# Kernel tuning notes

Measured on AMD Instinct MI355X. Metric: run time of the kernel, lower is better.

The kernel has to match this reference:

```python
import jax, jax.numpy as jnp
import numpy as np

# Model dims (match init_kwargs / input_specs)
L, D, H, F = 4, 1024, 16, 4096   # layers, d_model, heads, ffn hidden
B, S = 4, 1024                    # batch, seq_len
HD = D // H                       # head dim = 64
K = 8                             # context-mask band width (k=8, 2//k == 0)
LN_EPS = 1e-5


def setup_inputs():
    key = jax.random.key(0)
    ks = jax.random.split(key, 16)
    s = 0.02  # init scale for weights
    return {
        "src":   jax.random.normal(ks[0], (B, S, D), jnp.float32),
        # stacked per-layer params (leading dim L)
        "Wqkv":  jax.random.normal(ks[1], (L, 3 * D, D), jnp.float32) * s,
        "bqkv":  jnp.zeros((L, 3 * D), jnp.float32),
        "Wo":    jax.random.normal(ks[2], (L, D, D), jnp.float32) * s,
        "bo":    jnp.zeros((L, D), jnp.float32),
        "W1":    jax.random.normal(ks[3], (L, F, D), jnp.float32) * s,
        "b1":    jnp.zeros((L, F), jnp.float32),
        "W2":    jax.random.normal(ks[4], (L, D, F), jnp.float32) * s,
        "b2":    jnp.zeros((L, D), jnp.float32),
        "ln1_w": jnp.ones((L, D), jnp.float32),
        "ln1_b": jnp.zeros((L, D), jnp.float32),
        "ln2_w": jnp.ones((L, D), jnp.float32),
        "ln2_b": jnp.zeros((L, D), jnp.float32),
    }


def _layer_norm(x, g, b):
    m = jnp.mean(x, axis=-1, keepdims=True)
    v = jnp.mean(jnp.square(x - m), axis=-1, keepdims=True)
    return (x - m) * jax.lax.rsqrt(v + LN_EPS) * g + b


def _context_mask(sz):
    # row i allows keys j with i <= j < i + K (clamped into range); 0 allowed, -inf masked
    i = jnp.arange(sz)[:, None]
    j = jnp.arange(sz)[None, :]
    return jnp.where((j >= i) & (j < i + K), 0.0, -jnp.inf).astype(jnp.float32)


def reference(src, Wqkv, bqkv, Wo, bo, W1, b1, W2, b2, ln1_w, ln1_b, ln2_w, ln2_b):
    mask = _context_mask(S)  # [S, S] additive mask
    scale = 1.0 / jnp.sqrt(jnp.float32(HD))
    x = src  # [B, S, D] (batch-first; equivalent to torch's permute round-trip)
    for l in range(L):
        # --- self-attention (post-norm, dropout=0) ---
        qkv = jnp.einsum('bsd,ed->bse', x, Wqkv[l]) + bqkv[l]  # [B,S,3D]
        q, k, v = jnp.split(qkv, 3, axis=-1)
        q = q.reshape(B, S, H, HD).transpose(0, 2, 1, 3)  # [B,H,S,HD]
        k = k.reshape(B, S, H, HD).transpose(0, 2, 1, 3)
        v = v.reshape(B, S, H, HD).transpose(0, 2, 1, 3)
        scores = jnp.einsum('bhqd,bhkd->bhqk', q, k) * scale + mask
        attn = jax.nn.softmax(scores, axis=-1)
        o = jnp.einsum('bhqk,bhkd->bhqd', attn, v)
        o = o.transpose(0, 2, 1, 3).reshape(B, S, D)
        o = jnp.einsum('bsd,ed->bse', o, Wo[l]) + bo[l]
        x = _layer_norm(x + o, ln1_w[l], ln1_b[l])
        # --- feed-forward, exact (erf) gelu ---
        h = jax.nn.gelu(jnp.einsum('bsd,fd->bsf', x, W1[l]) + b1[l], approximate=False)
        h = jnp.einsum('bsf,df->bsd', h, W2[l]) + b2[l]
        x = _layer_norm(x + h, ln2_w[l], ln2_b[l])
    return x
```

## Files before the change

kernel.cpp:

```cpp
#include <hip/hip_runtime.h>

#define LNUM 4
#define DMODEL 1024
#define NHEAD 16
#define FDIM 4096
#define BATCH 4
#define SEQ 1024
#define HDIM 64
#define KBAND 8
#define MROWS (BATCH * SEQ)

typedef __attribute__((ext_vector_type(8))) __bf16 bf16x8;
typedef __attribute__((ext_vector_type(4))) float f32x4;

__device__ __forceinline__ unsigned short f2bf(float f) {
  unsigned int u = __builtin_bit_cast(unsigned int, f);
  u = u + 0x7fffu + ((u >> 16) & 1u);
  return (unsigned short)(u >> 16);
}
__device__ __forceinline__ float bf2f(unsigned short h) {
  unsigned int u = ((unsigned int)h) << 16;
  return __builtin_bit_cast(float, u);
}

#define GLOAD16(gp, lp)                                                        \
  __builtin_amdgcn_global_load_lds(                                            \
      (const __attribute__((address_space(1))) void*)(gp),                     \
      (__attribute__((address_space(3))) void*)(lp), 16, 0, 0)

__global__ __launch_bounds__(256) void cvt_bf16(const float* __restrict__ in,
                                                unsigned short* __restrict__ out,
                                                long n) {
  long i = ((long)blockIdx.x * 256 + threadIdx.x) * 4;
  if (i + 3 < n) {
    float4 v = *reinterpret_cast<const float4*>(in + i);
    ushort4 o;
    o.x = f2bf(v.x);
    o.y = f2bf(v.y);
    o.z = f2bf(v.z);
    o.w = f2bf(v.w);
    *reinterpret_cast<ushort4*>(out + i) = o;
  }
}

template <int EPI>
__global__ __launch_bounds__(256, 3) void gemm128(const unsigned short* __restrict__ A,
                                                  const unsigned short* __restrict__ W,
                                                  const float* __restrict__ bias,
                                                  unsigned short* __restrict__ Cout,
                                                  int Ndim, int Kdim, int Ks) {
  __shared__ unsigned short As[4096];
  __shared__ unsigned short Bs[4096];
  const int tid = threadIdx.x;
  const int wave = tid >> 6;
  const int lane = tid & 63;

  const int gx = gridDim.x, gy = gridDim.y;
  const int nwg = gx * gy;
  const int lin = blockIdx.x + blockIdx.y * gx;
  const int q8 = nwg >> 3, r8 = nwg & 7;
  const int xcd = lin & 7, cidx = lin >> 3;
  const int cbase = (xcd < r8) ? xcd * (q8 + 1) : r8 * (q8 + 1) + (xcd - r8) * q8;
  const int swz = cbase + cidx;
  const int bm0 = (swz % gy) * 128;
  const int bn0 = (swz / gy) * 128;
  const int kz0 = blockIdx.z * Ks;

  const int r0 = tid >> 2;
  const int c0 = (((tid & 3) ^ ((tid >> 2) & 3)) << 3);
  const unsigned short* gA = A + (size_t)(bm0 + r0) * Kdim + kz0 + c0;
  const unsigned short* gB = W + (size_t)(bn0 + r0) * Kdim + kz0 + c0;
  const size_t rowstep = (size_t)64 * Kdim;

  f32x4 acc[4][4] = {};

  const int wr = (wave >> 1) * 64;
  const int wc = (wave & 1) * 64;
  const int fr = lane & 15;
  const int kg = lane >> 4;
  const int kofs = ((kg ^ (fr & 3)) << 3);

  const int nt = Ks >> 5;
  for (int t = 0; t < nt; ++t) {
    GLOAD16(gA, &As[wave * 512]);
    GLOAD16(gA + rowstep, &As[2048 + wave * 512]);
    GLOAD16(gB, &Bs[wave * 512]);
    GLOAD16(gB + rowstep, &Bs[2048 + wave * 512]);
    gA += 32;
    gB += 32;
    __syncthreads();
    bf16x8 af[4], bfr[4];
#pragma unroll
    for (int i = 0; i < 4; ++i)
      af[i] = *reinterpret_cast<const bf16x8*>(&As[(wr + i * 16 + fr) * 32 + kofs]);
#pragma unroll
    for (int j = 0; j < 4; ++j)
      bfr[j] = *reinterpret_cast<const bf16x8*>(&Bs[(wc + j * 16 + fr) * 32 + kofs]);
#pragma unroll
    for (int i = 0; i < 4; ++i)
#pragma unroll
      for (int j = 0; j < 4; ++j)
        acc[i][j] = __builtin_amdgcn_mfma_f32_16x16x32_bf16(af[i], bfr[j], acc[i][j], 0, 0, 0);
    __syncthreads();
  }

  const int rr = (lane >> 4) * 4;
  const int cc = lane & 15;
  const bool addb = (EPI != 2) || (blockIdx.z == 0);
  unsigned short* outZ =
      Cout + (EPI == 2 ? (size_t)blockIdx.z * ((size_t)gy * 128) * Ndim : 0);
#pragma unroll
  for (int j = 0; j < 4; ++j) {
    const int n = bn0 + wc + j * 16 + cc;
    const float bv = addb ? bias[n] : 0.0f;
#pragma unroll
    for (int i = 0; i < 4; ++i) {
#pragma unroll
      for (int r = 0; r < 4; ++r) {
        const int m = bm0 + wr + i * 16 + rr + r;
        float v = acc[i][j][r] + bv;
        if (EPI == 1) v = 0.5f * v * (1.0f + erff(v * 0.70710678118654752f));
        outZ[(size_t)m * Ndim + n] = f2bf(v);
      }
    }
  }
}

__global__ __launch_bounds__(256) void attn_band(const unsigned short* __restrict__ qkv,
                                                 unsigned short* __restrict__ outp) {
  const int gw = blockIdx.x * 4 + (threadIdx.x >> 6);
  const int lane = threadIdx.x & 63;
  const int q = gw & (SEQ - 1);
  const int bh = gw >> 10;
  const int h = bh & (NHEAD - 1);
  const int b = bh >> 4;
  const size_t row0 = (size_t)(b * SEQ + q);
  const size_t stride = 3 * DMODEL;
  const float qv = bf2f(qkv[row0 * stride + h * HDIM + lane]);

  float sc[KBAND];
  float mx = -1e30f;
#pragma unroll
  for (int jj = 0; jj < KBAND; ++jj) {
    const int j = q + jj;
    const int jc = (j < SEQ) ? j : (SEQ - 1);
    float kv = bf2f(qkv[(size_t)(b * SEQ + jc) * stride + DMODEL + h * HDIM + lane]);
    float p = qv * kv;
#pragma unroll
    for (int m = 32; m; m >>= 1) p += __shfl_xor(p, m);
    p *= 0.125f;
    p = (j < SEQ) ? p : -1e30f;
    sc[jj] = p;
    mx = fmaxf(mx, p);
  }
  float denom = 0.f;
  float ov = 0.f;
#pragma unroll
  for (int jj = 0; jj < KBAND; ++jj) {
    const int j = q + jj;
    const int jc = (j < SEQ) ? j : (SEQ - 1);
    float p = __expf(sc[jj] - mx);
    p = (j < SEQ) ? p : 0.f;
    denom += p;
    ov += p * bf2f(qkv[(size_t)(b * SEQ + jc) * stride + 2 * DMODEL + h * HDIM + lane]);
  }
  ov /= denom;
  outp[row0 * DMODEL + h * HDIM + lane] = f2bf(ov);
}

__global__ __launch_bounds__(256) void add_ln2(const float* __restrict__ resid,
                                               const unsigned short* __restrict__ part,
                                               const float* __restrict__ gw,
                                               const float* __restrict__ gb,
                                               float* __restrict__ xf,
                                               unsigned short* __restrict__ xb) {
  const int row = blockIdx.x;
  const int tid = threadIdx.x;
  const size_t slab = (size_t)MROWS * DMODEL;
  const float* rp = resid + (size_t)row * DMODEL;
  const unsigned short* pp = part + (size_t)row * DMODEL;
  float v[4];
  float s = 0.f, s2 = 0.f;
#pragma unroll
  for (int i = 0; i < 4; ++i) {
    const int idx = tid + i * 256;
    float a = rp[idx] + bf2f(pp[idx]) + bf2f(pp[slab + idx]);
    v[i] = a;
    s += a;
    s2 += a * a;
  }
#pragma unroll
  for (int m = 32; m; m >>= 1) {
    s += __shfl_xor(s, m);
    s2 += __shfl_xor(s2, m);
  }
  __shared__ float wsm[8];
  const int wave = tid >> 6, lane = tid & 63;
  if (lane == 0) {
    wsm[wave] = s;
    wsm[4 + wave] = s2;
  }
  __syncthreads();
  s = wsm[0] + wsm[1] + wsm[2] + wsm[3];
  s2 = wsm[4] + wsm[5] + wsm[6] + wsm[7];
  const float mean = s * (1.f / DMODEL);
  const float var = s2 * (1.f / DMODEL) - mean * mean;
  const float rstd = rsqrtf(var + 1e-5f);
#pragma unroll
  for (int i = 0; i < 4; ++i) {
    const int idx = tid + i * 256;
    const float y = (v[i] - mean) * rstd * gw[idx] + gb[idx];
    xf[(size_t)row * DMODEL + idx] = y;
    xb[(size_t)row * DMODEL + idx] = f2bf(y);
  }
}

extern "C" void kernel_launch(void* const* d_in, const int* in_sizes, int n_in,
                              void* d_out, int out_size, void* d_ws, size_t ws_size,
                              hipStream_t stream) {
  const float* src  = (const float*)d_in[0];
  const float* Wqkv = (const float*)d_in[1];
  const float* bqkv = (const float*)d_in[2];
  const float* Wo   = (const float*)d_in[3];
  const float* bo   = (const float*)d_in[4];
  const float* W1   = (const float*)d_in[5];
  const float* b1   = (const float*)d_in[6];
  const float* W2   = (const float*)d_in[7];
  const float* b2   = (const float*)d_in[8];
  const float* ln1w = (const float*)d_in[9];
  const float* ln1b = (const float*)d_in[10];
  const float* ln2w = (const float*)d_in[11];
  const float* ln2b = (const float*)d_in[12];
  float* out = (float*)d_out;

  char* p = (char*)d_ws;
  unsigned short* wqkv_b = (unsigned short*)p; p += (size_t)LNUM * 3072 * 1024 * 2;
  unsigned short* wo_b   = (unsigned short*)p; p += (size_t)LNUM * 1024 * 1024 * 2;
  unsigned short* w1_b   = (unsigned short*)p; p += (size_t)LNUM * 4096 * 1024 * 2;
  unsigned short* w2_b   = (unsigned short*)p; p += (size_t)LNUM * 1024 * 4096 * 2;
  float*          xf     = (float*)p;          p += (size_t)MROWS * DMODEL * 4;
  unsigned short* xb     = (unsigned short*)p; p += (size_t)MROWS * DMODEL * 2;
  char* R = p;
  unsigned short* qkvb = (unsigned short*)R;
  unsigned short* aob  = (unsigned short*)(R + (size_t)MROWS * 3 * DMODEL * 2);
  unsigned short* hb   = (unsigned short*)R;
  unsigned short* part = (unsigned short*)(R + (size_t)MROWS * 4096 * 2);
  p = R + (size_t)MROWS * 4096 * 2 + (size_t)2 * MROWS * DMODEL * 2;
  if (ws_size < (size_t)(p - (char*)d_ws)) return;

  cvt_bf16<<<(long)LNUM * 3072 * 1024 / 1024, 256, 0, stream>>>(Wqkv, wqkv_b, (long)LNUM * 3072 * 1024);
  cvt_bf16<<<(long)LNUM * 1024 * 1024 / 1024, 256, 0, stream>>>(Wo, wo_b, (long)LNUM * 1024 * 1024);
  cvt_bf16<<<(long)LNUM * 4096 * 1024 / 1024, 256, 0, stream>>>(W1, w1_b, (long)LNUM * 4096 * 1024);
  cvt_bf16<<<(long)LNUM * 1024 * 4096 / 1024, 256, 0, stream>>>(W2, w2_b, (long)LNUM * 1024 * 4096);
  cvt_bf16<<<(long)MROWS * DMODEL / 1024, 256, 0, stream>>>(src, xb, (long)MROWS * DMODEL);

  for (int l = 0; l < LNUM; ++l) {
    gemm128<0><<<dim3(3072 / 128, MROWS / 128, 1), 256, 0, stream>>>(
        xb, wqkv_b + (size_t)l * 3072 * 1024, bqkv + l * 3072, qkvb, 3072, 1024, 1024);
    attn_band<<<(BATCH * NHEAD * SEQ) / 4, 256, 0, stream>>>(qkvb, aob);
    gemm128<2><<<dim3(1024 / 128, MROWS / 128, 2), 256, 0, stream>>>(
        aob, wo_b + (size_t)l * 1024 * 1024, bo + l * 1024, part, 1024, 1024, 512);
    add_ln2<<<MROWS, 256, 0, stream>>>(l == 0 ? src : xf, part,
                                       ln1w + l * DMODEL, ln1b + l * DMODEL, xf, xb);
    gemm128<1><<<dim3(FDIM / 128, MROWS / 128, 1), 256, 0, stream>>>(
        xb, w1_b + (size_t)l * 4096 * 1024, b1 + l * FDIM, hb, FDIM, 1024, 1024);
    gemm128<2><<<dim3(1024 / 128, MROWS / 128, 2), 256, 0, stream>>>(
        hb, w2_b + (size_t)l * 1024 * 4096, b2 + l * 1024, part, 1024, 4096, 2048);
    float* dst = (l == LNUM - 1) ? out : xf;
    add_ln2<<<MROWS, 256, 0, stream>>>(xf, part,
                                       ln2w + l * DMODEL, ln2b + l * DMODEL, dst, xb);
  }
}
```

Measured before the change: 961.8 us.

## Stage GEMM epilogue through LDS for vectorized stores and change LDS swizzle

The GEMM epilogue now writes each wave's results into a padded LDS tile and reads them back so every lane issues 16-byte global stores, replacing scattered 2-byte stores. The shared buffers are merged into one array so the epilogue can reuse them. The XOR swizzle for the A/B tiles also changes to use a different row bit pattern, aiming to reduce LDS bank conflicts on fragment reads. The LDS round trip adds latency and relies on waitcnt ordering within a wave, with no barrier between waves.

```diff
diff --git a/kernel.cpp b/kernel.cpp
--- a/kernel.cpp
+++ b/kernel.cpp
@@ -12,6 +12,7 @@
 
 typedef __attribute__((ext_vector_type(8))) __bf16 bf16x8;
 typedef __attribute__((ext_vector_type(4))) float f32x4;
+typedef __attribute__((ext_vector_type(8))) unsigned short u16x8;
 
 __device__ __forceinline__ unsigned short f2bf(float f) {
   unsigned int u = __builtin_bit_cast(unsigned int, f);
@@ -49,8 +50,9 @@
                                                   const float* __restrict__ bias,
                                                   unsigned short* __restrict__ Cout,
                                                   int Ndim, int Kdim, int Ks) {
-  __shared__ unsigned short As[4096];
-  __shared__ unsigned short Bs[4096];
+  __shared__ unsigned short SH[8192];
+  unsigned short* As = SH;
+  unsigned short* Bs = SH + 4096;
   const int tid = threadIdx.x;
   const int wave = tid >> 6;
   const int lane = tid & 63;
@@ -67,7 +69,7 @@
   const int kz0 = blockIdx.z * Ks;
 
   const int r0 = tid >> 2;
-  const int c0 = (((tid & 3) ^ ((tid >> 2) & 3)) << 3);
+  const int c0 = (((tid & 3) ^ ((tid >> 3) & 3)) << 3);
   const unsigned short* gA = A + (size_t)(bm0 + r0) * Kdim + kz0 + c0;
   const unsigned short* gB = W + (size_t)(bn0 + r0) * Kdim + kz0 + c0;
   const size_t rowstep = (size_t)64 * Kdim;
@@ -78,7 +80,7 @@
   const int wc = (wave & 1) * 64;
   const int fr = lane & 15;
   const int kg = lane >> 4;
-  const int kofs = ((kg ^ (fr & 3)) << 3);
+  const int kofs = ((kg ^ ((fr >> 1) & 3)) << 3);
 
   const int nt = Ks >> 5;
   for (int t = 0; t < nt; ++t) {
@@ -109,19 +111,37 @@
   const bool addb = (EPI != 2) || (blockIdx.z == 0);
   unsigned short* outZ =
       Cout + (EPI == 2 ? (size_t)blockIdx.z * ((size_t)gy * 128) * Ndim : 0);
-#pragma unroll
-  for (int j = 0; j < 4; ++j) {
-    const int n = bn0 + wc + j * 16 + cc;
-    const float bv = addb ? bias[n] : 0.0f;
-#pragma unroll
-    for (int i = 0; i < 4; ++i) {
-#pragma unroll
-      for (int r = 0; r < 4; ++r) {
-        const int m = bm0 + wr + i * 16 + rr + r;
-        float v = acc[i][j][r] + bv;
-        if (EPI == 1) v = 0.5f * v * (1.0f + erff(v * 0.70710678118654752f));
-        outZ[(size_t)m * Ndim + n] = f2bf(v);
-      }
+  float bv[4];
+#pragma unroll
+  for (int j = 0; j < 4; ++j)
+    bv[j] = addb ? bias[bn0 + wc + j * 16 + cc] : 0.0f;
+
+  unsigned short* lt = SH + wave * 1280;
+#pragma unroll
+  for (int rh = 0; rh < 2; ++rh) {
+#pragma unroll
+    for (int cp = 0; cp < 2; ++cp) {
+#pragma unroll
+      for (int ii = 0; ii < 2; ++ii)
+#pragma unroll
+        for (int jj = 0; jj < 2; ++jj)
+#pragma unroll
+          for (int r = 0; r < 4; ++r) {
+            float v = acc[rh * 2 + ii][cp * 2 + jj][r] + bv[cp * 2 + jj];
+            if (EPI == 1) v = 0.5f * v * (1.0f + erff(v * 0.70710678118654752f));
+            lt[(ii * 16 + rr + r) * 40 + jj * 16 + cc] = f2bf(v);
+          }
+      asm volatile("s_waitcnt lgkmcnt(0)" ::: "memory");
+      const int rl = lane >> 1;
+      const int chalf = (lane & 1) * 16;
+      u16x8 o0 = *reinterpret_cast<const u16x8*>(&lt[rl * 40 + chalf]);
+      u16x8 o1 = *reinterpret_cast<const u16x8*>(&lt[rl * 40 + chalf + 8]);
+      const int m = bm0 + wr + rh * 32 + rl;
+      const int n0 = bn0 + wc + cp * 32 + chalf;
+      unsigned short* dst = outZ + (size_t)m * Ndim + n0;
+      *reinterpret_cast<u16x8*>(dst) = o0;
+      *reinterpret_cast<u16x8*>(dst + 8) = o1;
+      asm volatile("s_waitcnt lgkmcnt(0)" ::: "memory");
     }
   }
 }
```

New measurement: 942.5 us. 1.02x faster.
